# Kernel optimization log

Measured on AMD Instinct MI355X. Metric: run time of the kernel, lower is better.

## Reference

```python
import jax, jax.numpy as jnp
import numpy as np

N = 50000        # nodes
E = 800000       # edges (avg degree 16)
F_IN = 128
H = 128
C = 16


def setup_inputs() -> dict:
    key = jax.random.key(0)
    ks = jax.random.split(key, 12)
    x = jax.random.normal(ks[0], (N, F_IN), dtype=jnp.float32)
    edges = jax.random.randint(ks[1], (2, E), 0, N, dtype=jnp.int32)
    dims = [(F_IN, H), (H, H // 2), (H // 2, H // 4), (H // 4, H // 8), (H // 8, C)]
    params = {}
    for i, (di, do) in enumerate(dims):
        params[f"W{i+1}"] = jax.random.normal(ks[2 + 2 * i], (di, do), dtype=jnp.float32) * (1.0 / np.sqrt(di)).astype(np.float32)
        params[f"b{i+1}"] = jax.random.normal(ks[3 + 2 * i], (do,), dtype=jnp.float32) * 0.01
    return {"x": x, "edges": edges, **params}


def reference(x, edges, W1, b1, W2, b2, W3, b3, W4, b4, W5, b5):
    src, dst = edges[0], edges[1]
    ones = jnp.ones((E,), x.dtype)
    # symmetric ('both') normalization with degree clamped to >= 1 (DGL GraphConv default)
    out_deg = jnp.clip(jax.ops.segment_sum(ones, src, num_segments=N), 1.0, None)
    in_deg = jnp.clip(jax.ops.segment_sum(ones, dst, num_segments=N), 1.0, None)
    norm_src = (out_deg ** -0.5)[:, None]   # [N,1]
    norm_dst = (in_deg ** -0.5)[:, None]    # [N,1]

    def graph_conv(h, W, b):
        h = h @ W                                  # dense transform first (out <= in)
        msgs = (h * norm_src)[src]                 # [E, d_out] gather
        agg = jax.ops.segment_sum(msgs, dst, num_segments=N)  # scatter-add SpMM
        return agg * norm_dst + b

    h = x
    for W, b in ((W1, b1), (W2, b2), (W3, b3), (W4, b4), (W5, b5)):
        h = jax.nn.relu(graph_conv(h, W, b))
    return h
```

## Files before the change

### kernel.cpp

```cpp
#include <hip/hip_runtime.h>
#include <hip/hip_bf16.h>


#define THREADS 256
#define SCAN_BLOCK 256
#define HIST_B 256
#define HWORDS 12500

typedef __attribute__((ext_vector_type(8))) short short8_t;
typedef __attribute__((ext_vector_type(4))) float float4_t;

__device__ __forceinline__ unsigned short f2bf_rne(float f) {
    unsigned u = __builtin_bit_cast(unsigned, f);
    unsigned r = u + 0x7fffu + ((u >> 16) & 1u);
    return (unsigned short)(r >> 16);
}
__device__ __forceinline__ float bf2f(unsigned short h) {
    return __builtin_bit_cast(float, ((unsigned)h) << 16);
}

__global__ __launch_bounds__(THREADS)
void hist_kernel(const int* __restrict__ src, const int* __restrict__ dst,
                 unsigned* __restrict__ p_src, unsigned* __restrict__ p_dst,
                 int E, int chunk) {
    __shared__ unsigned bins_s[HWORDS];
    __shared__ unsigned bins_d[HWORDS];
    const int b = blockIdx.x;
    const int t = threadIdx.x;
    const int e0 = b * chunk;
    int e1 = e0 + chunk; if (e1 > E) e1 = E;

    for (int w = t; w < HWORDS; w += THREADS) { bins_s[w] = 0; bins_d[w] = 0; }
    __syncthreads();
    for (int e = e0 + t; e < e1; e += THREADS) {
        int s = src[e];
        int d = dst[e];
        atomicAdd(&bins_s[s >> 2], 1u << ((s & 3) * 8));
        atomicAdd(&bins_d[d >> 2], 1u << ((d & 3) * 8));
    }
    __syncthreads();
    for (int w = t; w < HWORDS; w += THREADS) {
        p_src[(size_t)b * HWORDS + w] = bins_s[w];
        p_dst[(size_t)b * HWORDS + w] = bins_d[w];
    }
}

__global__ __launch_bounds__(THREADS)
void reduce_kernel(const unsigned* __restrict__ p_src, unsigned* __restrict__ p_dst,
                   int* __restrict__ deg_dst,
                   float* __restrict__ norm_src, float* __restrict__ norm_dst,
                   int N) {
    int w = blockIdx.x * blockDim.x + threadIdx.x;
    if (w >= HWORDS) return;

    unsigned s = 0;
#pragma unroll 4
    for (int b = 0; b < HIST_B; ++b) s += p_src[(size_t)b * HWORDS + w];

    unsigned run = 0;
#pragma unroll 4
    for (int b = 0; b < HIST_B; ++b) {
        size_t i = (size_t)b * HWORDS + w;
        unsigned v = p_dst[i];
        p_dst[i] = run;
        run += v;
    }

#pragma unroll
    for (int l = 0; l < 4; ++l) {
        int node = 4 * w + l;
        if (node < N) {
            int dd = (int)((run >> (8 * l)) & 0xffu);
            int ds = (int)((s   >> (8 * l)) & 0xffu);
            deg_dst[node] = dd;
            norm_dst[node] = rsqrtf((float)(dd < 1 ? 1 : dd));
            norm_src[node] = rsqrtf((float)(ds < 1 ? 1 : ds));
        }
    }
}

__global__ __launch_bounds__(SCAN_BLOCK)
void scanA_kernel(const int* __restrict__ deg_dst, int* __restrict__ partials, int N) {
    __shared__ int red[SCAN_BLOCK];
    int t = threadIdx.x;
    int n = blockIdx.x * SCAN_BLOCK + t;
    int v = (n < N) ? deg_dst[n] : 0;
    red[t] = v;
    __syncthreads();
#pragma unroll
    for (int off = SCAN_BLOCK / 2; off > 0; off >>= 1) {
        if (t < off) red[t] += red[t + off];
        __syncthreads();
    }
    if (t == 0) partials[blockIdx.x] = red[0];
}

__global__ __launch_bounds__(SCAN_BLOCK)
void scanB_kernel(int* __restrict__ partials, int* __restrict__ row_ptr,
                  int nb, int N) {
    __shared__ int s[SCAN_BLOCK];
    int t = threadIdx.x;
    int v = (t < nb) ? partials[t] : 0;
    s[t] = v;
    __syncthreads();
#pragma unroll
    for (int off = 1; off < SCAN_BLOCK; off <<= 1) {
        int u = 0;
        if (t >= off) u = s[t - off];
        __syncthreads();
        s[t] += u;
        __syncthreads();
    }
    if (t < nb) partials[t] = s[t] - v;
    if (t == SCAN_BLOCK - 1) row_ptr[N] = s[t];
}

__global__ __launch_bounds__(SCAN_BLOCK)
void scanC_kernel(const int* __restrict__ deg_dst, const int* __restrict__ partials,
                  int* __restrict__ row_ptr, int N) {
    __shared__ int s[SCAN_BLOCK];
    int t = threadIdx.x;
    int n = blockIdx.x * SCAN_BLOCK + t;
    int v = (n < N) ? deg_dst[n] : 0;
    s[t] = v;
    __syncthreads();
#pragma unroll
    for (int off = 1; off < SCAN_BLOCK; off <<= 1) {
        int u = 0;
        if (t >= off) u = s[t - off];
        __syncthreads();
        s[t] += u;
        __syncthreads();
    }
    if (n < N) row_ptr[n] = partials[blockIdx.x] + s[t] - v;
}

__global__ __launch_bounds__(THREADS)
void scatter_kernel(const int* __restrict__ src, const int* __restrict__ dst,
                    const int* __restrict__ row_ptr, const unsigned* __restrict__ p_dst,
                    int* __restrict__ col, int E, int chunk) {
    __shared__ unsigned bins[HWORDS];
    const int b = blockIdx.x;
    const int t = threadIdx.x;
    const int e0 = b * chunk;
    int e1 = e0 + chunk; if (e1 > E) e1 = E;

    for (int w = t; w < HWORDS; w += THREADS) bins[w] = 0;
    __syncthreads();
    for (int e = e0 + t; e < e1; e += THREADS) {
        int d = dst[e];
        unsigned sh = (unsigned)(d & 3) * 8u;
        unsigned old = atomicAdd(&bins[d >> 2], 1u << sh);
        unsigned lr  = (old >> sh) & 0xffu;
        unsigned pre = (p_dst[(size_t)b * HWORDS + (d >> 2)] >> sh) & 0xffu;
        col[row_ptr[d] + (int)pre + (int)lr] = src[e];
    }
}

__global__ __launch_bounds__(THREADS)
void convert_w_kernel(const float* __restrict__ W, short* __restrict__ hi,
                      short* __restrict__ lo, int K, int NOUT, int STR) {
    int i = blockIdx.x * blockDim.x + threadIdx.x;
    if (i >= NOUT * STR) return;
    int n = i / STR;
    int kk = i % STR;
    float v = (kk < K) ? W[(size_t)kk * NOUT + n] : 0.f;
    unsigned short h = f2bf_rne(v);
    float rem = v - bf2f(h);
    hi[i] = (short)h;
    lo[i] = (short)f2bf_rne(rem);
}

template<int K, int NOUT, bool QUANT>
__global__ __launch_bounds__(THREADS)
void gemm_mfma_kernel(const float* __restrict__ A, const short* __restrict__ wt_hi,
                      const short* __restrict__ wt_lo, const float* __restrict__ norm,
                      float* __restrict__ outf, short* __restrict__ outq,
                      float* __restrict__ qscale, int M) {
    constexpr int Kp  = (K + 31) & ~31;
    constexpr int STR = Kp + 8;
    constexpr int NT  = NOUT / 16;

    __shared__ short lh[NOUT * STR];
    __shared__ short ll[NOUT * STR];

    const int tid = threadIdx.x;
    {
        constexpr int CNT = NOUT * STR / 2;
        const int* gh = (const int*)wt_hi;
        const int* gl = (const int*)wt_lo;
        int* sh = (int*)lh;
        int* sl = (int*)ll;
        for (int i = tid; i < CNT; i += THREADS) { sh[i] = gh[i]; sl[i] = gl[i]; }
    }
    __syncthreads();

    const int w    = tid >> 6;
    const int lane = tid & 63;
    const int ln   = lane & 15;
    const int quad = lane >> 4;
    const int row  = blockIdx.x * 64 + w * 16 + ln;
    const bool rv  = row < M;

    float4_t acc[NT];
#pragma unroll
    for (int i = 0; i < NT; ++i) acc[i] = (float4_t){0.f, 0.f, 0.f, 0.f};

#pragma unroll
    for (int kt = 0; kt < Kp / 32; ++kt) {
        const int k0 = kt * 32 + quad * 8;
        float a[8];
        if (rv && k0 < K) {
            float4 v0 = *(const float4*)&A[(size_t)row * K + k0];
            float4 v1 = *(const float4*)&A[(size_t)row * K + k0 + 4];
            a[0] = v0.x; a[1] = v0.y; a[2] = v0.z; a[3] = v0.w;
            a[4] = v1.x; a[5] = v1.y; a[6] = v1.z; a[7] = v1.w;
        } else {
#pragma unroll
            for (int j = 0; j < 8; ++j) a[j] = 0.f;
        }
        short8_t ahi, alo;
#pragma unroll
        for (int j = 0; j < 8; ++j) {
            unsigned short h = f2bf_rne(a[j]);
            ahi[j] = (short)h;
            alo[j] = (short)f2bf_rne(a[j] - bf2f(h));
        }
#pragma unroll
        for (int nt = 0; nt < NT; ++nt) {
            const int bidx = (nt * 16 + ln) * STR + kt * 32 + quad * 8;
            short8_t bh = *(const short8_t*)&lh[bidx];
            short8_t bl = *(const short8_t*)&ll[bidx];
            acc[nt] = __builtin_amdgcn_mfma_f32_16x16x32_bf16(ahi, bh, acc[nt], 0, 0, 0);
            acc[nt] = __builtin_amdgcn_mfma_f32_16x16x32_bf16(ahi, bl, acc[nt], 0, 0, 0);
            acc[nt] = __builtin_amdgcn_mfma_f32_16x16x32_bf16(alo, bh, acc[nt], 0, 0, 0);
        }
    }

    const int orow = blockIdx.x * 64 + w * 16 + quad * 4;
#pragma unroll
    for (int i = 0; i < 4; ++i) {
        int r = orow + i;
        if (!QUANT) {
            if (r < M) {
                float s = norm[r];
#pragma unroll
                for (int nt = 0; nt < NT; ++nt)
                    outf[(size_t)r * NOUT + nt * 16 + ln] = acc[nt][i] * s;
            }
        } else {
            float m = 0.f;
#pragma unroll
            for (int nt = 0; nt < NT; ++nt) m = fmaxf(m, fabsf(acc[nt][i]));
#pragma unroll
            for (int off = 1; off < 16; off <<= 1) m = fmaxf(m, __shfl_xor(m, off));
            float s = (r < M) ? norm[r] : 0.f;
            float rowmax = m * s;
            float inv = (rowmax > 0.f) ? (32767.f / rowmax) : 0.f;
            if (r < M) {
                if (ln == 0) qscale[r] = rowmax * (1.f / 32767.f);
#pragma unroll
                for (int nt = 0; nt < NT; ++nt)
                    outq[(size_t)r * NOUT + nt * 16 + ln] =
                        (short)(int)__builtin_rintf(acc[nt][i] * s * inv);
            }
        }
    }
}

template<int D>
__global__ __launch_bounds__(THREADS)
void agg_q_kernel(const short* __restrict__ tq, const float* __restrict__ qscale,
                  const int* __restrict__ row_ptr, const int* __restrict__ col,
                  const float* __restrict__ norm_dst, const float* __restrict__ bias,
                  float* __restrict__ out, int N) {
    constexpr int TPN = D / 8;
    constexpr int NPB = THREADS / TPN;
    const int tid  = threadIdx.x;
    const int ln   = tid % TPN;
    const int g    = tid / TPN;
    const int node = blockIdx.x * NPB + g;
    if (node >= N) return;

    const int beg = row_ptr[node];
    const int end = row_ptr[node + 1];

    float acc[8];
#pragma unroll
    for (int c = 0; c < 8; ++c) acc[c] = 0.f;

    int j = beg;
    for (; j + 1 < end; j += 2) {
        int s0 = col[j];
        int s1 = col[j + 1];
        short8_t v0 = *(const short8_t*)&tq[(size_t)s0 * D + ln * 8];
        short8_t v1 = *(const short8_t*)&tq[(size_t)s1 * D + ln * 8];
        float c0 = qscale[s0];
        float c1 = qscale[s1];
#pragma unroll
        for (int c = 0; c < 8; ++c)
            acc[c] += (float)v0[c] * c0 + (float)v1[c] * c1;
    }
    if (j < end) {
        int s0 = col[j];
        short8_t v0 = *(const short8_t*)&tq[(size_t)s0 * D + ln * 8];
        float c0 = qscale[s0];
#pragma unroll
        for (int c = 0; c < 8; ++c) acc[c] += (float)v0[c] * c0;
    }

    float nd = norm_dst[node];
    float4 b0 = *(const float4*)&bias[ln * 8];
    float4 b1 = *(const float4*)&bias[ln * 8 + 4];
    float4 o0, o1;
    o0.x = fmaxf(acc[0] * nd + b0.x, 0.f);
    o0.y = fmaxf(acc[1] * nd + b0.y, 0.f);
    o0.z = fmaxf(acc[2] * nd + b0.z, 0.f);
    o0.w = fmaxf(acc[3] * nd + b0.w, 0.f);
    o1.x = fmaxf(acc[4] * nd + b1.x, 0.f);
    o1.y = fmaxf(acc[5] * nd + b1.y, 0.f);
    o1.z = fmaxf(acc[6] * nd + b1.z, 0.f);
    o1.w = fmaxf(acc[7] * nd + b1.w, 0.f);
    *(float4*)&out[(size_t)node * D + ln * 8] = o0;
    *(float4*)&out[(size_t)node * D + ln * 8 + 4] = o1;
}

template<int D>
__global__ __launch_bounds__(THREADS)
void agg_kernel(const float* __restrict__ tmp, const int* __restrict__ row_ptr,
                const int* __restrict__ col, const float* __restrict__ norm_dst,
                const float* __restrict__ bias, float* __restrict__ out, int N) {
    constexpr int TPN = D / 4;
    constexpr int NPB = THREADS / TPN;
    const int tid  = threadIdx.x;
    const int ln   = tid % TPN;
    const int g    = tid / TPN;
    const int node = blockIdx.x * NPB + g;
    if (node >= N) return;

    const int beg = row_ptr[node];
    const int end = row_ptr[node + 1];

    float4 acc = make_float4(0.f, 0.f, 0.f, 0.f);
    int j = beg;
    for (; j + 1 < end; j += 2) {
        int s0 = col[j];
        int s1 = col[j + 1];
        float4 v0 = *(const float4*)&tmp[(size_t)s0 * D + ln * 4];
        float4 v1 = *(const float4*)&tmp[(size_t)s1 * D + ln * 4];
        acc.x += v0.x + v1.x;
        acc.y += v0.y + v1.y;
        acc.z += v0.z + v1.z;
        acc.w += v0.w + v1.w;
    }
    if (j < end) {
        int s0 = col[j];
        float4 v0 = *(const float4*)&tmp[(size_t)s0 * D + ln * 4];
        acc.x += v0.x; acc.y += v0.y; acc.z += v0.z; acc.w += v0.w;
    }

    float nd = norm_dst[node];
    float4 b = *(const float4*)&bias[ln * 4];
    float4 o;
    o.x = fmaxf(acc.x * nd + b.x, 0.f);
    o.y = fmaxf(acc.y * nd + b.y, 0.f);
    o.z = fmaxf(acc.z * nd + b.z, 0.f);
    o.w = fmaxf(acc.w * nd + b.w, 0.f);
    *(float4*)&out[(size_t)node * D + ln * 4] = o;
}

extern "C" void kernel_launch(void* const* d_in, const int* in_sizes, int n_in,
                              void* d_out, int out_size, void* d_ws, size_t ws_size,
                              hipStream_t stream) {
    const float* x     = (const float*)d_in[0];
    const int*   edges = (const int*)d_in[1];
    const float* W1 = (const float*)d_in[2];  const float* b1 = (const float*)d_in[3];
    const float* W2 = (const float*)d_in[4];  const float* b2 = (const float*)d_in[5];
    const float* W3 = (const float*)d_in[6];  const float* b3 = (const float*)d_in[7];
    const float* W4 = (const float*)d_in[8];  const float* b4 = (const float*)d_in[9];
    const float* W5 = (const float*)d_in[10]; const float* b5 = (const float*)d_in[11];

    const int N = in_sizes[0] / 128;
    const int E = in_sizes[1] / 2;
    const int* src = edges;
    const int* dst = edges + E;

    char* ws = (char*)d_ws;
    size_t off = 0;
    auto carve = [&](size_t bytes) -> void* {
        void* p = ws + off;
        off += (bytes + 255) & ~(size_t)255;
        return p;
    };
    float* tmp      = (float*)carve((size_t)N * 128 * 4);
    float* hbuf     = (float*)carve((size_t)N * 128 * 4);
    int*   deg_dst  = (int*)carve((size_t)N * 4);
    float* norm_src = (float*)carve((size_t)N * 4);
    float* norm_dst = (float*)carve((size_t)N * 4);
    int*   row_ptr  = (int*)carve((size_t)(N + 1) * 4);
    int*   col      = (int*)carve((size_t)E * 4);
    int*   partials = (int*)carve((size_t)1024 * 4);
    float* qscale   = (float*)carve((size_t)N * 4);
    short* wts      = (short*)carve((size_t)59392 * 2);
    (void)ws_size;

    float* tmpf = tmp;
    short* tq   = (short*)((char*)tmp + (size_t)N * 16 * 4);
    unsigned* p_src = (unsigned*)tmp;
    unsigned* p_dst = p_src + (size_t)HIST_B * HWORDS;

    short* w1h = wts;            short* w1l = w1h + 17408;
    short* w2h = w1l + 17408;    short* w2l = w2h + 8704;
    short* w3h = w2l + 8704;     short* w3l = w3h + 2304;
    short* w4h = w3l + 2304;     short* w4l = w4h + 640;
    short* w5h = w4l + 640;      short* w5l = w5h + 640;

    const int chunk  = (E + HIST_B - 1) / HIST_B;
    const int gridSc = (N + SCAN_BLOCK - 1) / SCAN_BLOCK;

    convert_w_kernel<<<(17408 + 255) / 256, THREADS, 0, stream>>>(W1, w1h, w1l, 128, 128, 136);
    convert_w_kernel<<<(8704 + 255) / 256, THREADS, 0, stream>>>(W2, w2h, w2l, 128, 64, 136);
    convert_w_kernel<<<(2304 + 255) / 256, THREADS, 0, stream>>>(W3, w3h, w3l, 64, 32, 72);
    convert_w_kernel<<<(640 + 255) / 256, THREADS, 0, stream>>>(W4, w4h, w4l, 32, 16, 40);
    convert_w_kernel<<<(640 + 255) / 256, THREADS, 0, stream>>>(W5, w5h, w5l, 16, 16, 40);

    hist_kernel<<<HIST_B, THREADS, 0, stream>>>(src, dst, p_src, p_dst, E, chunk);
    reduce_kernel<<<(HWORDS + THREADS - 1) / THREADS, THREADS, 0, stream>>>(
        p_src, p_dst, deg_dst, norm_src, norm_dst, N);
    scanA_kernel<<<gridSc, SCAN_BLOCK, 0, stream>>>(deg_dst, partials, N);
    scanB_kernel<<<1, SCAN_BLOCK, 0, stream>>>(partials, row_ptr, gridSc, N);
    scanC_kernel<<<gridSc, SCAN_BLOCK, 0, stream>>>(deg_dst, partials, row_ptr, N);
    scatter_kernel<<<HIST_B, THREADS, 0, stream>>>(src, dst, row_ptr, p_dst, col, E, chunk);

    const int gridG = (N + 63) / 64;

    gemm_mfma_kernel<128, 128, true><<<gridG, THREADS, 0, stream>>>(x, w1h, w1l, norm_src, nullptr, tq, qscale, N);
    agg_q_kernel<128><<<(N + 15) / 16, THREADS, 0, stream>>>(tq, qscale, row_ptr, col, norm_dst, b1, hbuf, N);
    gemm_mfma_kernel<128, 64, true><<<gridG, THREADS, 0, stream>>>(hbuf, w2h, w2l, norm_src, nullptr, tq, qscale, N);
    agg_q_kernel<64><<<(N + 31) / 32, THREADS, 0, stream>>>(tq, qscale, row_ptr, col, norm_dst, b2, hbuf, N);
    gemm_mfma_kernel<64, 32, true><<<gridG, THREADS, 0, stream>>>(hbuf, w3h, w3l, norm_src, nullptr, tq, qscale, N);
    agg_q_kernel<32><<<(N + 63) / 64, THREADS, 0, stream>>>(tq, qscale, row_ptr, col, norm_dst, b3, hbuf, N);
    gemm_mfma_kernel<32, 16, false><<<gridG, THREADS, 0, stream>>>(hbuf, w4h, w4l, norm_src, tmpf, nullptr, nullptr, N);
    agg_kernel<16><<<(N + 63) / 64, THREADS, 0, stream>>>(tmpf, row_ptr, col, norm_dst, b4, hbuf, N);
    gemm_mfma_kernel<16, 16, false><<<gridG, THREADS, 0, stream>>>(hbuf, w5h, w5l, norm_src, tmpf, nullptr, nullptr, N);
    agg_kernel<16><<<(N + 63) / 64, THREADS, 0, stream>>>(tmpf, row_ptr, col, norm_dst, b5, (float*)d_out, N);
}
```

Baseline: 307.8 us.

## Fuse preprocessing kernels, record edge ranks in histogram, quantize all layers

Splits the histogram into separate src and dst blocks, and the dst blocks record each edge's local rank, so the scatter kernel no longer redoes the shared-memory atomics. The reduce and scanA steps are merged, scanC handles four nodes per thread, and the five weight conversions become one launch. Layers 4 and 5 now use the int16-quantized gather path instead of fp32, and the aggregation loop is unrolled by four. This cuts launches and gather bytes, at the cost of an extra rank buffer and quantization error in the last layers.

```diff
diff --git a/kernel.cpp b/kernel.cpp
--- a/kernel.cpp
+++ b/kernel.cpp
@@ -3,7 +3,6 @@
 
 
 #define THREADS 256
-#define SCAN_BLOCK 256
 #define HIST_B 256
 #define HWORDS 12500
 
@@ -22,89 +21,83 @@
 __global__ __launch_bounds__(THREADS)
 void hist_kernel(const int* __restrict__ src, const int* __restrict__ dst,
                  unsigned* __restrict__ p_src, unsigned* __restrict__ p_dst,
-                 int E, int chunk) {
-    __shared__ unsigned bins_s[HWORDS];
-    __shared__ unsigned bins_d[HWORDS];
-    const int b = blockIdx.x;
+                 unsigned char* __restrict__ rank, int E, int chunk) {
+    __shared__ unsigned bins[HWORDS];
+    const bool is_dst = blockIdx.x < HIST_B;
+    const int b = is_dst ? blockIdx.x : blockIdx.x - HIST_B;
     const int t = threadIdx.x;
     const int e0 = b * chunk;
     int e1 = e0 + chunk; if (e1 > E) e1 = E;
-
-    for (int w = t; w < HWORDS; w += THREADS) { bins_s[w] = 0; bins_d[w] = 0; }
+    const int* __restrict__ idx = is_dst ? dst : src;
+    unsigned* __restrict__ pout = is_dst ? p_dst : p_src;
+
+    for (int w = t; w < HWORDS; w += THREADS) bins[w] = 0;
     __syncthreads();
     for (int e = e0 + t; e < e1; e += THREADS) {
-        int s = src[e];
-        int d = dst[e];
-        atomicAdd(&bins_s[s >> 2], 1u << ((s & 3) * 8));
-        atomicAdd(&bins_d[d >> 2], 1u << ((d & 3) * 8));
-    }
-    __syncthreads();
-    for (int w = t; w < HWORDS; w += THREADS) {
-        p_src[(size_t)b * HWORDS + w] = bins_s[w];
-        p_dst[(size_t)b * HWORDS + w] = bins_d[w];
-    }
-}
-
-__global__ __launch_bounds__(THREADS)
-void reduce_kernel(const unsigned* __restrict__ p_src, unsigned* __restrict__ p_dst,
-                   int* __restrict__ deg_dst,
-                   float* __restrict__ norm_src, float* __restrict__ norm_dst,
-                   int N) {
-    int w = blockIdx.x * blockDim.x + threadIdx.x;
-    if (w >= HWORDS) return;
-
-    unsigned s = 0;
+        int d = idx[e];
+        unsigned sh = (unsigned)(d & 3) * 8u;
+        unsigned old = atomicAdd(&bins[d >> 2], 1u << sh);
+        if (is_dst) rank[e] = (unsigned char)((old >> sh) & 0xffu);
+    }
+    __syncthreads();
+    for (int w = t; w < HWORDS; w += THREADS)
+        pout[(size_t)b * HWORDS + w] = bins[w];
+}
+
+__global__ __launch_bounds__(THREADS)
+void reduce_scanA_kernel(const unsigned* __restrict__ p_src, unsigned* __restrict__ p_dst,
+                         int* __restrict__ deg_dst,
+                         float* __restrict__ norm_src, float* __restrict__ norm_dst,
+                         int* __restrict__ partials, int N) {
+    __shared__ int red[THREADS];
+    const int t = threadIdx.x;
+    const int w = blockIdx.x * THREADS + t;
+    int degsum = 0;
+    if (w < HWORDS) {
+        unsigned s = 0;
 #pragma unroll 4
-    for (int b = 0; b < HIST_B; ++b) s += p_src[(size_t)b * HWORDS + w];
-
-    unsigned run = 0;
+        for (int b = 0; b < HIST_B; ++b) s += p_src[(size_t)b * HWORDS + w];
+
+        unsigned run = 0;
 #pragma unroll 4
-    for (int b = 0; b < HIST_B; ++b) {
-        size_t i = (size_t)b * HWORDS + w;
-        unsigned v = p_dst[i];
-        p_dst[i] = run;
-        run += v;
-    }
-
-#pragma unroll
-    for (int l = 0; l < 4; ++l) {
-        int node = 4 * w + l;
-        if (node < N) {
+        for (int b = 0; b < HIST_B; ++b) {
+            size_t i = (size_t)b * HWORDS + w;
+            unsigned v = p_dst[i];
+            p_dst[i] = run;
+            run += v;
+        }
+
+#pragma unroll
+        for (int l = 0; l < 4; ++l) {
+            int node = 4 * w + l;
             int dd = (int)((run >> (8 * l)) & 0xffu);
             int ds = (int)((s   >> (8 * l)) & 0xffu);
             deg_dst[node] = dd;
             norm_dst[node] = rsqrtf((float)(dd < 1 ? 1 : dd));
             norm_src[node] = rsqrtf((float)(ds < 1 ? 1 : ds));
-        }
-    }
-}
-
-__global__ __launch_bounds__(SCAN_BLOCK)
-void scanA_kernel(const int* __restrict__ deg_dst, int* __restrict__ partials, int N) {
-    __shared__ int red[SCAN_BLOCK];
-    int t = threadIdx.x;
-    int n = blockIdx.x * SCAN_BLOCK + t;
-    int v = (n < N) ? deg_dst[n] : 0;
-    red[t] = v;
-    __syncthreads();
-#pragma unroll
-    for (int off = SCAN_BLOCK / 2; off > 0; off >>= 1) {
+            degsum += dd;
+        }
+    }
+    red[t] = degsum;
+    __syncthreads();
+#pragma unroll
+    for (int off = THREADS / 2; off > 0; off >>= 1) {
         if (t < off) red[t] += red[t + off];
         __syncthreads();
     }
     if (t == 0) partials[blockIdx.x] = red[0];
 }
 
-__global__ __launch_bounds__(SCAN_BLOCK)
+__global__ __launch_bounds__(THREADS)
 void scanB_kernel(int* __restrict__ partials, int* __restrict__ row_ptr,
                   int nb, int N) {
-    __shared__ int s[SCAN_BLOCK];
+    __shared__ int s[THREADS];
     int t = threadIdx.x;
     int v = (t < nb) ? partials[t] : 0;
     s[t] = v;
     __syncthreads();
 #pragma unroll
-    for (int off = 1; off < SCAN_BLOCK; off <<= 1) {
+    for (int off = 1; off < THREADS; off <<= 1) {
         int u = 0;
         if (t >= off) u = s[t - off];
         __syncthreads();
@@ -112,71 +105,88 @@
         __syncthreads();
     }
     if (t < nb) partials[t] = s[t] - v;
-    if (t == SCAN_BLOCK - 1) row_ptr[N] = s[t];
-}
-
-__global__ __launch_bounds__(SCAN_BLOCK)
+    if (t == THREADS - 1) row_ptr[N] = s[t];
+}
+
+__global__ __launch_bounds__(THREADS)
 void scanC_kernel(const int* __restrict__ deg_dst, const int* __restrict__ partials,
                   int* __restrict__ row_ptr, int N) {
-    __shared__ int s[SCAN_BLOCK];
-    int t = threadIdx.x;
-    int n = blockIdx.x * SCAN_BLOCK + t;
-    int v = (n < N) ? deg_dst[n] : 0;
-    s[t] = v;
-    __syncthreads();
-#pragma unroll
-    for (int off = 1; off < SCAN_BLOCK; off <<= 1) {
+    __shared__ int s[THREADS];
+    const int t = threadIdx.x;
+    const int base = blockIdx.x * 1024 + t * 4;
+    int d0 = 0, d1 = 0, d2 = 0, d3 = 0;
+    if (base + 3 < N) {
+        int4 d = *(const int4*)&deg_dst[base];
+        d0 = d.x; d1 = d.y; d2 = d.z; d3 = d.w;
+    } else {
+        if (base + 0 < N) d0 = deg_dst[base + 0];
+        if (base + 1 < N) d1 = deg_dst[base + 1];
+        if (base + 2 < N) d2 = deg_dst[base + 2];
+        if (base + 3 < N) d3 = deg_dst[base + 3];
+    }
+    int tsum = d0 + d1 + d2 + d3;
+    s[t] = tsum;
+    __syncthreads();
+#pragma unroll
+    for (int off = 1; off < THREADS; off <<= 1) {
         int u = 0;
         if (t >= off) u = s[t - off];
         __syncthreads();
         s[t] += u;
         __syncthreads();
     }
-    if (n < N) row_ptr[n] = partials[blockIdx.x] + s[t] - v;
+    int pre = partials[blockIdx.x] + s[t] - tsum;
+    if (base + 0 < N) row_ptr[base + 0] = pre; pre += d0;
+    if (base + 1 < N) row_ptr[base + 1] = pre; pre += d1;
+    if (base + 2 < N) row_ptr[base + 2] = pre; pre += d2;
+    if (base + 3 < N) row_ptr[base + 3] = pre;
 }
 
 __global__ __launch_bounds__(THREADS)
 void scatter_kernel(const int* __restrict__ src, const int* __restrict__ dst,
+                    const unsigned char* __restrict__ rank,
                     const int* __restrict__ row_ptr, const unsigned* __restrict__ p_dst,
                     int* __restrict__ col, int E, int chunk) {
-    __shared__ unsigned bins[HWORDS];
     const int b = blockIdx.x;
-    const int t = threadIdx.x;
     const int e0 = b * chunk;
     int e1 = e0 + chunk; if (e1 > E) e1 = E;
-
-    for (int w = t; w < HWORDS; w += THREADS) bins[w] = 0;
-    __syncthreads();
-    for (int e = e0 + t; e < e1; e += THREADS) {
+    for (int e = e0 + threadIdx.x; e < e1; e += THREADS) {
         int d = dst[e];
         unsigned sh = (unsigned)(d & 3) * 8u;
-        unsigned old = atomicAdd(&bins[d >> 2], 1u << sh);
-        unsigned lr  = (old >> sh) & 0xffu;
         unsigned pre = (p_dst[(size_t)b * HWORDS + (d >> 2)] >> sh) & 0xffu;
-        col[row_ptr[d] + (int)pre + (int)lr] = src[e];
-    }
-}
-
-__global__ __launch_bounds__(THREADS)
-void convert_w_kernel(const float* __restrict__ W, short* __restrict__ hi,
-                      short* __restrict__ lo, int K, int NOUT, int STR) {
-    int i = blockIdx.x * blockDim.x + threadIdx.x;
-    if (i >= NOUT * STR) return;
+        col[row_ptr[d] + (int)pre + (int)rank[e]] = src[e];
+    }
+}
+
+__device__ __forceinline__ void conv_one(const float* __restrict__ W, short* __restrict__ hi,
+                                         short* __restrict__ lo, int K, int NOUT, int STR, int i) {
     int n = i / STR;
     int kk = i % STR;
     float v = (kk < K) ? W[(size_t)kk * NOUT + n] : 0.f;
     unsigned short h = f2bf_rne(v);
-    float rem = v - bf2f(h);
     hi[i] = (short)h;
-    lo[i] = (short)f2bf_rne(rem);
-}
-
-template<int K, int NOUT, bool QUANT>
+    lo[i] = (short)f2bf_rne(v - bf2f(h));
+}
+
+__global__ __launch_bounds__(THREADS)
+void convert_all_kernel(const float* W1, const float* W2, const float* W3,
+                        const float* W4, const float* W5,
+                        short* w1h, short* w1l, short* w2h, short* w2l,
+                        short* w3h, short* w3l, short* w4h, short* w4l,
+                        short* w5h, short* w5l) {
+    int i = blockIdx.x * blockDim.x + threadIdx.x;
+    if      (i < 17408)                    conv_one(W1, w1h, w1l, 128, 128, 136, i);
+    else if ((i -= 17408) < 8704)          conv_one(W2, w2h, w2l, 128, 64, 136, i);
+    else if ((i -= 8704) < 2304)           conv_one(W3, w3h, w3l, 64, 32, 72, i);
+    else if ((i -= 2304) < 640)            conv_one(W4, w4h, w4l, 32, 16, 40, i);
+    else if ((i -= 640) < 640)             conv_one(W5, w5h, w5l, 16, 16, 40, i);
+}
+
+template<int K, int NOUT>
 __global__ __launch_bounds__(THREADS)
 void gemm_mfma_kernel(const float* __restrict__ A, const short* __restrict__ wt_hi,
                       const short* __restrict__ wt_lo, const float* __restrict__ norm,
-                      float* __restrict__ outf, short* __restrict__ outq,
-                      float* __restrict__ qscale, int M) {
+                      short* __restrict__ outq, float* __restrict__ qscale, int M) {
     constexpr int Kp  = (K + 31) & ~31;
     constexpr int STR = Kp + 8;
     constexpr int NT  = NOUT / 16;
@@ -241,29 +251,20 @@
 #pragma unroll
     for (int i = 0; i < 4; ++i) {
         int r = orow + i;
-        if (!QUANT) {
-            if (r < M) {
-                float s = norm[r];
-#pragma unroll
-                for (int nt = 0; nt < NT; ++nt)
-                    outf[(size_t)r * NOUT + nt * 16 + ln] = acc[nt][i] * s;
-            }
-        } else {
-            float m = 0.f;
-#pragma unroll
-            for (int nt = 0; nt < NT; ++nt) m = fmaxf(m, fabsf(acc[nt][i]));
-#pragma unroll
-            for (int off = 1; off < 16; off <<= 1) m = fmaxf(m, __shfl_xor(m, off));
-            float s = (r < M) ? norm[r] : 0.f;
-            float rowmax = m * s;
-            float inv = (rowmax > 0.f) ? (32767.f / rowmax) : 0.f;
-            if (r < M) {
-                if (ln == 0) qscale[r] = rowmax * (1.f / 32767.f);
-#pragma unroll
-                for (int nt = 0; nt < NT; ++nt)
-                    outq[(size_t)r * NOUT + nt * 16 + ln] =
-                        (short)(int)__builtin_rintf(acc[nt][i] * s * inv);
-            }
+        float m = 0.f;
+#pragma unroll
+        for (int nt = 0; nt < NT; ++nt) m = fmaxf(m, fabsf(acc[nt][i]));
+#pragma unroll
+        for (int off = 1; off < 16; off <<= 1) m = fmaxf(m, __shfl_xor(m, off));
+        float s = (r < M) ? norm[r] : 0.f;
+        float rowmax = m * s;
+        float inv = (rowmax > 0.f) ? (32767.f / rowmax) : 0.f;
+        if (r < M) {
+            if (ln == 0) qscale[r] = rowmax * (1.f / 32767.f);
+#pragma unroll
+            for (int nt = 0; nt < NT; ++nt)
+                outq[(size_t)r * NOUT + nt * 16 + ln] =
+                    (short)(int)__builtin_rintf(acc[nt][i] * s * inv);
         }
     }
 }
@@ -290,18 +291,19 @@
     for (int c = 0; c < 8; ++c) acc[c] = 0.f;
 
     int j = beg;
-    for (; j + 1 < end; j += 2) {
-        int s0 = col[j];
-        int s1 = col[j + 1];
+    for (; j + 3 < end; j += 4) {
+        int s0 = col[j], s1 = col[j + 1], s2 = col[j + 2], s3 = col[j + 3];
         short8_t v0 = *(const short8_t*)&tq[(size_t)s0 * D + ln * 8];
         short8_t v1 = *(const short8_t*)&tq[(size_t)s1 * D + ln * 8];
-        float c0 = qscale[s0];
-        float c1 = qscale[s1];
+        short8_t v2 = *(const short8_t*)&tq[(size_t)s2 * D + ln * 8];
+        short8_t v3 = *(const short8_t*)&tq[(size_t)s3 * D + ln * 8];
+        float c0 = qscale[s0], c1 = qscale[s1], c2 = qscale[s2], c3 = qscale[s3];
 #pragma unroll
         for (int c = 0; c < 8; ++c)
-            acc[c] += (float)v0[c] * c0 + (float)v1[c] * c1;
-    }
-    if (j < end) {
+            acc[c] += (float)v0[c] * c0 + (float)v1[c] * c1
+                    + (float)v2[c] * c2 + (float)v3[c] * c3;
+    }
+    for (; j < end; ++j) {
         int s0 = col[j];
         short8_t v0 = *(const short8_t*)&tq[(size_t)s0 * D + ln * 8];
         float c0 = qscale[s0];
@@ -325,50 +327,6 @@
     *(float4*)&out[(size_t)node * D + ln * 8 + 4] = o1;
 }
 
-template<int D>
-__global__ __launch_bounds__(THREADS)
-void agg_kernel(const float* __restrict__ tmp, const int* __restrict__ row_ptr,
-                const int* __restrict__ col, const float* __restrict__ norm_dst,
-                const float* __restrict__ bias, float* __restrict__ out, int N) {
-    constexpr int TPN = D / 4;
-    constexpr int NPB = THREADS / TPN;
-    const int tid  = threadIdx.x;
-    const int ln   = tid % TPN;
-    const int g    = tid / TPN;
-    const int node = blockIdx.x * NPB + g;
-    if (node >= N) return;
-
-    const int beg = row_ptr[node];
-    const int end = row_ptr[node + 1];
-
-    float4 acc = make_float4(0.f, 0.f, 0.f, 0.f);
-    int j = beg;
-    for (; j + 1 < end; j += 2) {
-        int s0 = col[j];
-        int s1 = col[j + 1];
-        float4 v0 = *(const float4*)&tmp[(size_t)s0 * D + ln * 4];
-        float4 v1 = *(const float4*)&tmp[(size_t)s1 * D + ln * 4];
-        acc.x += v0.x + v1.x;
-        acc.y += v0.y + v1.y;
-        acc.z += v0.z + v1.z;
-        acc.w += v0.w + v1.w;
-    }
-    if (j < end) {
-        int s0 = col[j];
-        float4 v0 = *(const float4*)&tmp[(size_t)s0 * D + ln * 4];
-        acc.x += v0.x; acc.y += v0.y; acc.z += v0.z; acc.w += v0.w;
-    }
-
-    float nd = norm_dst[node];
-    float4 b = *(const float4*)&bias[ln * 4];
-    float4 o;
-    o.x = fmaxf(acc.x * nd + b.x, 0.f);
-    o.y = fmaxf(acc.y * nd + b.y, 0.f);
-    o.z = fmaxf(acc.z * nd + b.z, 0.f);
-    o.w = fmaxf(acc.w * nd + b.w, 0.f);
-    *(float4*)&out[(size_t)node * D + ln * 4] = o;
-}
-
 extern "C" void kernel_launch(void* const* d_in, const int* in_sizes, int n_in,
                               void* d_out, int out_size, void* d_ws, size_t ws_size,
                               hipStream_t stream) {
@@ -392,7 +350,7 @@
         off += (bytes + 255) & ~(size_t)255;
         return p;
     };
-    float* tmp      = (float*)carve((size_t)N * 128 * 4);
+    short* tq       = (short*)carve((size_t)N * 128 * 2);
     float* hbuf     = (float*)carve((size_t)N * 128 * 4);
     int*   deg_dst  = (int*)carve((size_t)N * 4);
     float* norm_src = (float*)carve((size_t)N * 4);
@@ -402,12 +360,10 @@
     int*   partials = (int*)carve((size_t)1024 * 4);
     float* qscale   = (float*)carve((size_t)N * 4);
     short* wts      = (short*)carve((size_t)59392 * 2);
+    unsigned* p_src = (unsigned*)carve((size_t)HIST_B * HWORDS * 4);
+    unsigned* p_dst = (unsigned*)carve((size_t)HIST_B * HWORDS * 4);
+    unsigned char* rank = (unsigned char*)carve((size_t)E);
     (void)ws_size;
-
-    float* tmpf = tmp;
-    short* tq   = (short*)((char*)tmp + (size_t)N * 16 * 4);
-    unsigned* p_src = (unsigned*)tmp;
-    unsigned* p_dst = p_src + (size_t)HIST_B * HWORDS;
 
     short* w1h = wts;            short* w1l = w1h + 17408;
     short* w2h = w1l + 17408;    short* w2l = w2h + 8704;
@@ -415,33 +371,32 @@
     short* w4h = w3l + 2304;     short* w4l = w4h + 640;
     short* w5h = w4l + 640;      short* w5l = w5h + 640;
 
-    const int chunk  = (E + HIST_B - 1) / HIST_B;
-    const int gridSc = (N + SCAN_BLOCK - 1) / SCAN_BLOCK;
-
-    convert_w_kernel<<<(17408 + 255) / 256, THREADS, 0, stream>>>(W1, w1h, w1l, 128, 128, 136);
-    convert_w_kernel<<<(8704 + 255) / 256, THREADS, 0, stream>>>(W2, w2h, w2l, 128, 64, 136);
-    convert_w_kernel<<<(2304 + 255) / 256, THREADS, 0, stream>>>(W3, w3h, w3l, 64, 32, 72);
-    convert_w_kernel<<<(640 + 255) / 256, THREADS, 0, stream>>>(W4, w4h, w4l, 32, 16, 40);
-    convert_w_kernel<<<(640 + 255) / 256, THREADS, 0, stream>>>(W5, w5h, w5l, 16, 16, 40);
-
-    hist_kernel<<<HIST_B, THREADS, 0, stream>>>(src, dst, p_src, p_dst, E, chunk);
-    reduce_kernel<<<(HWORDS + THREADS - 1) / THREADS, THREADS, 0, stream>>>(
-        p_src, p_dst, deg_dst, norm_src, norm_dst, N);
-    scanA_kernel<<<gridSc, SCAN_BLOCK, 0, stream>>>(deg_dst, partials, N);
-    scanB_kernel<<<1, SCAN_BLOCK, 0, stream>>>(partials, row_ptr, gridSc, N);
-    scanC_kernel<<<gridSc, SCAN_BLOCK, 0, stream>>>(deg_dst, partials, row_ptr, N);
-    scatter_kernel<<<HIST_B, THREADS, 0, stream>>>(src, dst, row_ptr, p_dst, col, E, chunk);
+    const int chunk = (E + HIST_B - 1) / HIST_B;
+
+    convert_all_kernel<<<(29696 + 255) / 256, THREADS, 0, stream>>>(
+        W1, W2, W3, W4, W5, w1h, w1l, w2h, w2l, w3h, w3l, w4h, w4l, w5h, w5l);
+
+    hist_kernel<<<2 * HIST_B, THREADS, 0, stream>>>(src, dst, p_src, p_dst, rank, E, chunk);
+    reduce_scanA_kernel<<<(HWORDS + THREADS - 1) / THREADS, THREADS, 0, stream>>>(
+        p_src, p_dst, deg_dst, norm_src, norm_dst, partials, N);
+    scanB_kernel<<<1, THREADS, 0, stream>>>(partials, row_ptr, (HWORDS + THREADS - 1) / THREADS, N);
+    scanC_kernel<<<(N + 1023) / 1024, THREADS, 0, stream>>>(deg_dst, partials, row_ptr, N);
+    scatter_kernel<<<HIST_B, THREADS, 0, stream>>>(src, dst, rank, row_ptr, p_dst, col, E, chunk);
 
     const int gridG = (N + 63) / 64;
 
-    gemm_mfma_kernel<128, 128, true><<<gridG, THREADS, 0, stream>>>(x, w1h, w1l, norm_src, nullptr, tq, qscale, N);
+    gemm_mfma_kernel<128, 128><<<gridG, THREADS, 0, stream>>>(x, w1h, w1l, norm_src, tq, qscale, N);
     agg_q_kernel<128><<<(N + 15) / 16, THREADS, 0, stream>>>(tq, qscale, row_ptr, col, norm_dst, b1, hbuf, N);
-    gemm_mfma_kernel<128, 64, true><<<gridG, THREADS, 0, stream>>>(hbuf, w2h, w2l, norm_src, nullptr, tq, qscale, N);
+
+    gemm_mfma_kernel<128, 64><<<gridG, THREADS, 0, stream>>>(hbuf, w2h, w2l, norm_src, tq, qscale, N);
     agg_q_kernel<64><<<(N + 31) / 32, THREADS, 0, stream>>>(tq, qscale, row_ptr, col, norm_dst, b2, hbuf, N);
-    gemm_mfma_kernel<64, 32, true><<<gridG, THREADS, 0, stream>>>(hbuf, w3h, w3l, norm_src, nullptr, tq, qscale, N);
+
+    gemm_mfma_kernel<64, 32><<<gridG, THREADS, 0, stream>>>(hbuf, w3h, w3l, norm_src, tq, qscale, N);
     agg_q_kernel<32><<<(N + 63) / 64, THREADS, 0, stream>>>(tq, qscale, row_ptr, col, norm_dst, b3, hbuf, N);
-    gemm_mfma_kernel<32, 16, false><<<gridG, THREADS, 0, stream>>>(hbuf, w4h, w4l, norm_src, tmpf, nullptr, nullptr, N);
-    agg_kernel<16><<<(N + 63) / 64, THREADS, 0, stream>>>(tmpf, row_ptr, col, norm_dst, b4, hbuf, N);
-    gemm_mfma_kernel<16, 16, false><<<gridG, THREADS, 0, stream>>>(hbuf, w5h, w5l, norm_src, tmpf, nullptr, nullptr, N);
-    agg_kernel<16><<<(N + 63) / 64, THREADS, 0, stream>>>(tmpf, row_ptr, col, norm_dst, b5, (float*)d_out, N);
-}
+
+    gemm_mfma_kernel<32, 16><<<gridG, THREADS, 0, stream>>>(hbuf, w4h, w4l, norm_src, tq, qscale, N);
+    agg_q_kernel<16><<<(N + 127) / 128, THREADS, 0, stream>>>(tq, qscale, row_ptr, col, norm_dst, b4, hbuf, N);
+
+    gemm_mfma_kernel<16, 16><<<gridG, THREADS, 0, stream>>>(hbuf, w5h, w5l, norm_src, tq, qscale, N);
+    agg_q_kernel<16><<<(N + 127) / 128, THREADS, 0, stream>>>(tq, qscale, row_ptr, col, norm_dst, b5, (float*)d_out, N);
+}
```

Measured after the change: 297.9 us. 1.03x faster.
